# Performance work log

Hardware: AMD Instinct MI355X
Metric: run time of the kernel (lower is better)

The kernel has to match this reference:

```python
import jax, jax.numpy as jnp
import numpy as np

# Geometry constants fixed by the source's index arithmetic
GRID_P, GRID_Q, NUM_ANCH = 60, 40, 9   # p = (i//9)%60, q = i//(60*9), sr = i%9
N = GRID_P * GRID_Q * NUM_ANCH          # 21600 anchors per image
K = 1000                                # top-K candidates kept before NMS
MAX_BOXES = 18                          # fixed output boxes per image
THRESH = 0.5                            # NMS overlap threshold
BATCH = 64


def setup_inputs() -> dict:
    key = jax.random.key(0)
    k1, k2 = jax.random.split(key)
    x = jax.random.normal(k1, (BATCH, N, 6), dtype=jnp.float32)
    # anchor boxes (x, y, w, h); keep w,h strictly positive and away from 0
    anchor_boxes = jax.random.uniform(k2, (GRID_P, GRID_Q, NUM_ANCH, 4),
                                      dtype=jnp.float32, minval=0.05, maxval=1.0)
    return {"x": x, "anchor_boxes": anchor_boxes}


def _per_sample(ypred, anchors):
    scores, order = jax.lax.top_k(ypred[:, 0], K)          # descending, matches tf.argsort DESC [:1000]
    p = (order // NUM_ANCH) % GRID_P
    q = order // (GRID_P * NUM_ANCH)
    sr = order % NUM_ANCH
    a = anchors[p, q, sr]                                   # [K, 4] (xa, ya, wa, ha)
    regr = ypred[order, 2:6]                                # [K, 4] (dx, dy, dw, dh)
    xc = regr[:, 0] * a[:, 2] + a[:, 0]
    yc = regr[:, 1] * a[:, 3] + a[:, 1]
    w = a[:, 2] * jnp.exp(regr[:, 2])
    h = a[:, 3] * jnp.exp(regr[:, 3])
    cand = jnp.stack([xc, yc, w, h, scores], axis=-1)       # [K, 5] xywh+score

    # xywh -> xyxy for overlap computation (as in non_max_suppression_fast)
    x1 = xc - 0.5 * w; x2 = xc + 0.5 * w
    y1 = yc - 0.5 * h; y2 = yc + 0.5 * h
    area = (x2 - x1) * (y2 - y1)                            # [K]

    # pairwise intersection; overlap[i, j] = inter(i, j) / area(j)  (source divides by
    # the area of the lower-scored candidate, NOT the union -- kept faithfully)
    xx1 = jnp.maximum(x1[:, None], x1[None, :])
    yy1 = jnp.maximum(y1[:, None], y1[None, :])
    xx2 = jnp.minimum(x2[:, None], x2[None, :])
    yy2 = jnp.minimum(y2[:, None], y2[None, :])
    iw = jnp.maximum(0.0, xx2 - xx1)
    ih = jnp.maximum(0.0, yy2 - yy1)
    sup = (iw * ih / area[None, :]) > THRESH                # [K, K] bool

    # greedy NMS over candidates in descending-score order
    jrange = jnp.arange(K)
    def body(i, keep):
        return keep & ~(keep[i] & sup[i] & (jrange > i))
    keep = jax.lax.fori_loop(0, K, body, jnp.ones((K,), dtype=bool))

    # pack first MAX_BOXES kept boxes into fixed-shape output
    ranks = jnp.cumsum(keep) - 1                            # position among kept
    valid = keep & (ranks < MAX_BOXES)
    picked = jnp.zeros((MAX_BOXES, 5), cand.dtype).at[
        jnp.where(valid, ranks, MAX_BOXES)
    ].set(jnp.where(valid[:, None], cand, 0.0), mode='drop')

    # pad with top-scored decoded boxes if fewer than MAX_BOXES survive NMS
    n = jnp.minimum(jnp.sum(keep), MAX_BOXES)
    j = jnp.arange(MAX_BOXES)
    pad = cand[jnp.clip(j - n, 0, K - 1)]
    return jnp.where((j < n)[:, None], picked, pad)         # [MAX_BOXES, 5]


def reference(x, anchor_boxes):
    return jax.vmap(lambda y: _per_sample(y, anchor_boxes))(x)  # [B, 18, 5]
```

## Files before the change

kernel.cpp:

```cpp
#include <hip/hip_runtime.h>

#define NELEM 21600
#define KSEL 1000
#define MAXB 18
#define NT 1024
#define CAP 2048
#define NCHUNK 4
#define CHUNK (NELEM / NCHUNK)
#define NFULL 21
#define NTAIL (NELEM - NFULL * NT)

typedef unsigned long long ull;

__device__ __forceinline__ unsigned fkey(float f) {
  unsigned u = __float_as_uint(f);
  return (u & 0x80000000u) ? ~u : (u | 0x80000000u);
}
__device__ __forceinline__ float unfkey(unsigned k) {
  unsigned u = (k & 0x80000000u) ? (k ^ 0x80000000u) : ~k;
  return __uint_as_float(u);
}

__global__ __launch_bounds__(NT) void k1_scan(
    const float* __restrict__ x, unsigned* __restrict__ gkeys,
    unsigned* __restrict__ ghist) {
  const int blk = blockIdx.x;
  const int s = blk / NCHUNK, c = blk % NCHUNK;
  const int t = threadIdx.x;
  const float* xb = x + (size_t)s * NELEM * 6;

  __shared__ unsigned h[2048];
  h[2 * t] = 0u; h[2 * t + 1] = 0u;
  __syncthreads();

  const int base = c * CHUNK;
  unsigned key[6];
  bool on[6];
  #pragma unroll
  for (int k = 0; k < 6; ++k) {
    int o = t + (k << 10);
    on[k] = o < CHUNK;
    int e = base + (on[k] ? o : 0);
    key[k] = fkey(xb[(size_t)e * 6]);
  }
  #pragma unroll
  for (int k = 0; k < 6; ++k) {
    if (on[k]) {
      int e = base + t + (k << 10);
      gkeys[(size_t)s * NELEM + e] = key[k];
      atomicAdd(&h[key[k] >> 21], 1u);
    }
  }
  __syncthreads();
  unsigned* gh = ghist + (size_t)blk * 2048;
  gh[2 * t] = h[2 * t];
  gh[2 * t + 1] = h[2 * t + 1];
}

__device__ void select_bucket(const unsigned* hist, unsigned target,
                              volatile unsigned* chunkSuf,
                              unsigned* outB, unsigned* outCnt, unsigned* outAbove) {
  const int tid = threadIdx.x;
  const int w = tid >> 6, l = tid & 63;
  unsigned h1 = hist[w * 128 + 2 * l + 1];
  unsigned s = hist[w * 128 + 2 * l] + h1;
  #pragma unroll
  for (int d = 1; d < 64; d <<= 1) {
    unsigned t = __shfl_down(s, d);
    if (l + d < 64) s += t;
  }
  if (l == 0) chunkSuf[w] = s;
  __syncthreads();
  if (w == 0) {
    unsigned ct = (l < 16) ? chunkSuf[l] : 0u;
    unsigned cs = ct;
    #pragma unroll
    for (int d = 1; d < 16; d <<= 1) {
      unsigned t = __shfl_down(cs, d);
      if (l + d < 16) cs += t;
    }
    if (l < 16) chunkSuf[l] = cs - ct;
  }
  __syncthreads();
  unsigned base = chunkSuf[w];
  unsigned sufE = s + base;
  unsigned sN = __shfl_down(s, 1);
  unsigned sufN = ((l < 63) ? sN : 0u) + base;
  unsigned geOdd = sufN + h1;
  if (sufE >= target && geOdd < target) { *outB = w * 128u + 2u * l;     *outCnt = sufE;  *outAbove = geOdd; }
  if (geOdd >= target && sufN < target) { *outB = w * 128u + 2u * l + 1; *outCnt = geOdd; *outAbove = sufN;  }
  __syncthreads();
}

__global__ __launch_bounds__(NT, 4) void k2_select(
    const float* __restrict__ x, const float* __restrict__ anch,
    const unsigned* __restrict__ gkeys, const unsigned* __restrict__ ghist,
    float* __restrict__ out) {
  const int s = blockIdx.x;
  const int tid = threadIdx.x;
  const float* xb = x + (size_t)s * NELEM * 6;
  const unsigned* ks = gkeys + (size_t)s * NELEM;

  __shared__ unsigned hist[2048];
  __shared__ unsigned chunkSuf[16];
  __shared__ ull selPk[CAP];
  __shared__ float bX1[KSEL], bY1[KSEL], bX2[KSEL], bY2[KSEL], bAr[KSEL];
  __shared__ unsigned sB, sCnt, sAbove;
  __shared__ unsigned baseKey;
  __shared__ unsigned cnt;
  __shared__ int keptRank[MAXB];
  __shared__ int numKept;

  unsigned kv[NFULL];
  #pragma unroll
  for (int u = 0; u < NFULL; ++u) kv[u] = ks[tid + (u << 10)];
  unsigned ktail = 0u;
  const bool hastail = tid < NTAIL;
  if (hastail) ktail = ks[tid + NFULL * NT];
  asm volatile("" :
      "+v"(kv[0]), "+v"(kv[1]), "+v"(kv[2]), "+v"(kv[3]), "+v"(kv[4]),
      "+v"(kv[5]), "+v"(kv[6]), "+v"(kv[7]), "+v"(kv[8]), "+v"(kv[9]),
      "+v"(kv[10]), "+v"(kv[11]), "+v"(kv[12]), "+v"(kv[13]), "+v"(kv[14]),
      "+v"(kv[15]), "+v"(kv[16]), "+v"(kv[17]), "+v"(kv[18]), "+v"(kv[19]),
      "+v"(kv[20]), "+v"(ktail));

  {
    unsigned h0 = 0, h1 = 0;
    #pragma unroll
    for (int c = 0; c < NCHUNK; ++c) {
      const unsigned* gh = ghist + (size_t)(s * NCHUNK + c) * 2048;
      h0 += gh[2 * tid];
      h1 += gh[2 * tid + 1];
    }
    hist[2 * tid] = h0; hist[2 * tid + 1] = h1;
  }
  __syncthreads();
  select_bucket(hist, KSEL, chunkSuf, &sB, &sCnt, &sAbove);
  const unsigned b1 = sB, cnt1 = sCnt, above1 = sAbove;

  if (cnt1 <= CAP) {
    if (tid == 0) { baseKey = b1 << 21; cnt = 0u; }
  } else {
    hist[2 * tid] = 0u; hist[2 * tid + 1] = 0u;
    __syncthreads();
    #pragma unroll
    for (int u = 0; u < NFULL; ++u)
      if ((kv[u] >> 21) == b1) atomicAdd(&hist[(kv[u] >> 10) & 0x7FFu], 1u);
    if (hastail && (ktail >> 21) == b1) atomicAdd(&hist[(ktail >> 10) & 0x7FFu], 1u);
    __syncthreads();
    select_bucket(hist, KSEL - above1, chunkSuf, &sB, &sCnt, &sAbove);
    if (tid == 0) { baseKey = (b1 << 21) | (sB << 10); cnt = 0u; }
  }
  __syncthreads();

  const unsigned TB = baseKey;
  #pragma unroll
  for (int u = 0; u < NFULL; ++u) {
    if (kv[u] >= TB) {
      unsigned p = atomicAdd(&cnt, 1u);
      unsigned i = (unsigned)(tid + (u << 10));
      if (p < CAP) selPk[p] = ((ull)kv[u] << 32) | (unsigned)(~i);
    }
  }
  if (hastail && ktail >= TB) {
    unsigned p = atomicAdd(&cnt, 1u);
    unsigned i = (unsigned)(tid + NFULL * NT);
    if (p < CAP) selPk[p] = ((ull)ktail << 32) | (unsigned)(~i);
  }
  __syncthreads();
  const unsigned realCnt = (cnt < CAP) ? cnt : CAP;
  for (unsigned i = realCnt + tid; i < CAP; i += NT) selPk[i] = 0ull;
  __syncthreads();

  {
    const int w = tid >> 6, L = tid & 63;
    const int ea = (w << 7) | (L << 1);
    ull a = selPk[ea], bb = selPk[ea + 1];
    #pragma unroll
    for (unsigned k = 2; k <= 128; k <<= 1) {
      #pragma unroll
      for (unsigned j = k >> 1; j >= 2; j >>= 1) {
        bool up = ((ea & k) == 0);
        bool lower = ((ea & j) == 0);
        bool takeMax = (up == lower);
        ull oa = __shfl_xor(a, (int)(j >> 1));
        ull ob = __shfl_xor(bb, (int)(j >> 1));
        a  = takeMax ? (a  > oa ? a  : oa) : (a  < oa ? a  : oa);
        bb = takeMax ? (bb > ob ? bb : ob) : (bb < ob ? bb : ob);
      }
      bool up = ((ea & k) == 0);
      ull mx = a > bb ? a : bb, mn = a > bb ? bb : a;
      a = up ? mx : mn; bb = up ? mn : mx;
    }
    selPk[ea] = a; selPk[ea + 1] = bb;
    __syncthreads();
    for (unsigned k = 256; k <= 2048; k <<= 1) {
      for (unsigned j = k >> 1; j >= 128; j >>= 1) {
        unsigned p = (unsigned)tid;
        unsigned vi = ((p & ~(j - 1)) << 1) | (p & (j - 1));
        unsigned li = vi | j;
        ull av = selPk[vi], cv = selPk[li];
        bool doswap = ((vi & k) == 0) ? (av < cv) : (av > cv);
        if (doswap) { selPk[vi] = cv; selPk[li] = av; }
        __syncthreads();
      }
      a = selPk[ea]; bb = selPk[ea + 1];
      bool up = (((unsigned)(w << 7) & k) == 0);
      #pragma unroll
      for (unsigned j = 64; j >= 2; j >>= 1) {
        bool lower = ((ea & j) == 0);
        bool takeMax = (up == lower);
        ull oa = __shfl_xor(a, (int)(j >> 1));
        ull ob = __shfl_xor(bb, (int)(j >> 1));
        a  = takeMax ? (a  > oa ? a  : oa) : (a  < oa ? a  : oa);
        bb = takeMax ? (bb > ob ? bb : ob) : (bb < ob ? bb : ob);
      }
      ull mx = a > bb ? a : bb, mn = a > bb ? bb : a;
      a = up ? mx : mn; bb = up ? mn : mx;
      selPk[ea] = a; selPk[ea + 1] = bb;
      __syncthreads();
    }
  }

  if (tid < KSEL) {
    unsigned idx = ~(unsigned)selPk[tid];
    const float2* e2 = (const float2*)(xb + (size_t)idx * 6 + 2);
    float2 ra = e2[0], rb = e2[1];
    unsigned pp = (idx / 9u) % 60u;
    unsigned qq = idx / 540u;
    unsigned sr = idx % 9u;
    const float* ap = anch + (((pp * 40u + qq) * 9u + sr) * 4u);
    float ax = ap[0], ay = ap[1], aw = ap[2], ah = ap[3];
    float xc = ra.x * aw + ax;
    float yc = ra.y * ah + ay;
    float w = aw * expf(rb.x);
    float h = ah * expf(rb.y);
    float x1 = xc - 0.5f * w, x2 = xc + 0.5f * w;
    float y1 = yc - 0.5f * h, y2 = yc + 0.5f * h;
    bX1[tid] = x1; bY1[tid] = y1; bX2[tid] = x2; bY2[tid] = y2;
    bAr[tid] = (x2 - x1) * (y2 - y1);
  }
  __syncthreads();

  if (tid < 64) {
    const int lane = tid;
    int nk = 0;
    float kx1 = 0.f, ky1 = 0.f, kx2 = 0.f, ky2 = 0.f;
    int krank = -1;
    for (int base = 0; base < KSEL && nk < MAXB; base += 64) {
      int c = base + lane;
      bool alive = (c < KSEL);
      int cc = alive ? c : 0;
      float x1 = bX1[cc], y1 = bY1[cc], x2 = bX2[cc], y2 = bY2[cc], ar = bAr[cc];
      for (int i = 0; i < nk; ++i) {
        float px1 = __shfl(kx1, i), py1 = __shfl(ky1, i);
        float px2 = __shfl(kx2, i), py2 = __shfl(ky2, i);
        float iw = fmaxf(fminf(x2, px2) - fmaxf(x1, px1), 0.f);
        float ih = fmaxf(fminf(y2, py2) - fmaxf(y1, py1), 0.f);
        if (iw * ih / ar > 0.5f) alive = false;
      }
      unsigned long long m = __ballot(alive);
      while (m) {
        int i = __builtin_ctzll(m);
        float px1 = __shfl(x1, i), py1 = __shfl(y1, i);
        float px2 = __shfl(x2, i), py2 = __shfl(y2, i);
        if (lane == nk) { kx1 = px1; ky1 = py1; kx2 = px2; ky2 = py2; krank = base + i; }
        ++nk;
        if (nk >= MAXB) break;
        if (alive && lane != i) {
          float iw = fmaxf(fminf(x2, px2) - fmaxf(x1, px1), 0.f);
          float ih = fmaxf(fminf(y2, py2) - fmaxf(y1, py1), 0.f);
          if (iw * ih / ar > 0.5f) alive = false;
        }
        if (lane == i) alive = false;
        m = __ballot(alive);
      }
    }
    if (lane == 0) numKept = nk;
    if (lane < nk) keptRank[lane] = krank;
  }
  __syncthreads();

  const int n = numKept;
  if (tid < MAXB) {
    int j = tid;
    int r = (j < n) ? keptRank[j] : (j - n);
    ull pk = selPk[r];
    unsigned idx = ~(unsigned)pk;
    float sc = unfkey((unsigned)(pk >> 32));
    const float2* e2 = (const float2*)(xb + (size_t)idx * 6 + 2);
    float2 ra = e2[0], rb = e2[1];
    unsigned pp = (idx / 9u) % 60u;
    unsigned qq = idx / 540u;
    unsigned sr = idx % 9u;
    const float* ap = anch + (((pp * 40u + qq) * 9u + sr) * 4u);
    float ax = ap[0], ay = ap[1], aw = ap[2], ah = ap[3];
    float xc = ra.x * aw + ax;
    float yc = ra.y * ah + ay;
    float w = aw * expf(rb.x);
    float h = ah * expf(rb.y);
    float* o = out + s * (MAXB * 5) + j * 5;
    o[0] = xc; o[1] = yc; o[2] = w; o[3] = h; o[4] = sc;
  }
}

extern "C" void kernel_launch(void* const* d_in, const int* in_sizes, int n_in,
                              void* d_out, int out_size, void* d_ws, size_t ws_size,
                              hipStream_t stream) {
  const float* x = (const float*)d_in[0];
  const float* anch = (const float*)d_in[1];
  float* out = (float*)d_out;
  const int B = in_sizes[0] / (NELEM * 6);
  unsigned* ghist = (unsigned*)d_ws;
  unsigned* gkeys = ghist + (size_t)B * NCHUNK * 2048;
  k1_scan<<<dim3(B * NCHUNK), dim3(NT), 0, stream>>>(x, gkeys, ghist);
  k2_select<<<dim3(B), dim3(NT), 0, stream>>>(x, anch, gkeys, ghist, out);
}
```

Measured before the change: 65.66 us.

## Aggregate compaction atomics per wave, add 1024-wide sort path, rework NMS loop

Compaction now uses one wave-level atomicAdd per ballot instead of a per-element atomic. The second-level histogram refinement is triggered above 1024 candidates so a smaller single-element-per-thread bitonic sort can run over 1024 entries, with an intra-wave shuffle phase and shared-memory phases. The NMS phase is rewritten so each lane holds 16 consecutive candidates in registers and the next kept box is found by a wave-wide min reduction; each kept box is then tested against all survivors. This trades extra histogram passes and more per-iteration register work for fewer atomics and less sort traffic.

```diff
diff --git a/kernel.cpp b/kernel.cpp
--- a/kernel.cpp
+++ b/kernel.cpp
@@ -138,9 +138,7 @@
   select_bucket(hist, KSEL, chunkSuf, &sB, &sCnt, &sAbove);
   const unsigned b1 = sB, cnt1 = sCnt, above1 = sAbove;
 
-  if (cnt1 <= CAP) {
-    if (tid == 0) { baseKey = b1 << 21; cnt = 0u; }
-  } else {
+  if (cnt1 > 1024) {
     hist[2 * tid] = 0u; hist[2 * tid + 1] = 0u;
     __syncthreads();
     #pragma unroll
@@ -150,16 +148,28 @@
     __syncthreads();
     select_bucket(hist, KSEL - above1, chunkSuf, &sB, &sCnt, &sAbove);
     if (tid == 0) { baseKey = (b1 << 21) | (sB << 10); cnt = 0u; }
+  } else {
+    if (tid == 0) { baseKey = b1 << 21; cnt = 0u; }
   }
   __syncthreads();
 
   const unsigned TB = baseKey;
+  const int lw = tid & 63;
   #pragma unroll
   for (int u = 0; u < NFULL; ++u) {
-    if (kv[u] >= TB) {
-      unsigned p = atomicAdd(&cnt, 1u);
-      unsigned i = (unsigned)(tid + (u << 10));
-      if (p < CAP) selPk[p] = ((ull)kv[u] << 32) | (unsigned)(~i);
+    bool pred = kv[u] >= TB;
+    ull mask = __ballot(pred);
+    if (mask) {
+      int leader = __builtin_ctzll(mask);
+      unsigned total = (unsigned)__popcll(mask);
+      unsigned basep = 0;
+      if (lw == leader) basep = atomicAdd(&cnt, total);
+      basep = __shfl(basep, leader);
+      if (pred) {
+        unsigned p = basep + (unsigned)__popcll(mask & ((1ull << lw) - 1ull));
+        unsigned i = (unsigned)(tid + (u << 10));
+        if (p < CAP) selPk[p] = ((ull)kv[u] << 32) | (unsigned)(~i);
+      }
     }
   }
   if (hastail && ktail >= TB) {
@@ -169,10 +179,52 @@
   }
   __syncthreads();
   const unsigned realCnt = (cnt < CAP) ? cnt : CAP;
-  for (unsigned i = realCnt + tid; i < CAP; i += NT) selPk[i] = 0ull;
-  __syncthreads();
-
-  {
+  const unsigned P = (realCnt <= 1024u) ? 1024u : 2048u;
+  for (unsigned i = realCnt + tid; i < P; i += NT) selPk[i] = 0ull;
+  __syncthreads();
+
+  if (P == 1024u) {
+    ull a = selPk[tid];
+    #pragma unroll
+    for (unsigned k = 2; k <= 64; k <<= 1) {
+      #pragma unroll
+      for (unsigned j = k >> 1; j >= 1; j >>= 1) {
+        bool up = ((tid & k) == 0);
+        bool lower = ((tid & j) == 0);
+        bool takeMax = (up == lower);
+        ull o = __shfl_xor(a, (int)j);
+        a = takeMax ? (a > o ? a : o) : (a < o ? a : o);
+      }
+    }
+    selPk[tid] = a;
+    __syncthreads();
+    for (unsigned k = 128; k <= 1024; k <<= 1) {
+      for (unsigned j = k >> 1; j >= 64; j >>= 1) {
+        if (tid < 512) {
+          unsigned p = (unsigned)tid;
+          unsigned vi = ((p & ~(j - 1)) << 1) | (p & (j - 1));
+          unsigned li = vi | j;
+          ull av = selPk[vi], cv = selPk[li];
+          bool doswap = ((vi & k) == 0) ? (av < cv) : (av > cv);
+          if (doswap) { selPk[vi] = cv; selPk[li] = av; }
+        }
+        __syncthreads();
+      }
+      a = selPk[tid];
+      {
+        bool up = ((tid & k) == 0);
+        #pragma unroll
+        for (unsigned j = 32; j >= 1; j >>= 1) {
+          bool lower = ((tid & j) == 0);
+          bool takeMax = (up == lower);
+          ull o = __shfl_xor(a, (int)j);
+          a = takeMax ? (a > o ? a : o) : (a < o ? a : o);
+        }
+      }
+      selPk[tid] = a;
+      __syncthreads();
+    }
+  } else {
     const int w = tid >> 6, L = tid & 63;
     const int ea = (w << 7) | (L << 1);
     ull a = selPk[ea], bb = selPk[ea + 1];
@@ -244,40 +296,42 @@
 
   if (tid < 64) {
     const int lane = tid;
+    float X1[16], Y1[16], X2[16], Y2[16], AR[16];
+    unsigned alive = 0u;
+    #pragma unroll
+    for (int ss = 0; ss < 16; ++ss) {
+      int r = lane * 16 + ss;
+      bool ok = r < KSEL;
+      int rr = ok ? r : 0;
+      X1[ss] = bX1[rr]; Y1[ss] = bY1[rr];
+      X2[ss] = bX2[rr]; Y2[ss] = bY2[rr]; AR[ss] = bAr[rr];
+      alive |= (ok ? 1u : 0u) << ss;
+    }
     int nk = 0;
-    float kx1 = 0.f, ky1 = 0.f, kx2 = 0.f, ky2 = 0.f;
-    int krank = -1;
-    for (int base = 0; base < KSEL && nk < MAXB; base += 64) {
-      int c = base + lane;
-      bool alive = (c < KSEL);
-      int cc = alive ? c : 0;
-      float x1 = bX1[cc], y1 = bY1[cc], x2 = bX2[cc], y2 = bY2[cc], ar = bAr[cc];
-      for (int i = 0; i < nk; ++i) {
-        float px1 = __shfl(kx1, i), py1 = __shfl(ky1, i);
-        float px2 = __shfl(kx2, i), py2 = __shfl(ky2, i);
-        float iw = fmaxf(fminf(x2, px2) - fmaxf(x1, px1), 0.f);
-        float ih = fmaxf(fminf(y2, py2) - fmaxf(y1, py1), 0.f);
-        if (iw * ih / ar > 0.5f) alive = false;
-      }
-      unsigned long long m = __ballot(alive);
-      while (m) {
-        int i = __builtin_ctzll(m);
-        float px1 = __shfl(x1, i), py1 = __shfl(y1, i);
-        float px2 = __shfl(x2, i), py2 = __shfl(y2, i);
-        if (lane == nk) { kx1 = px1; ky1 = py1; kx2 = px2; ky2 = py2; krank = base + i; }
-        ++nk;
-        if (nk >= MAXB) break;
-        if (alive && lane != i) {
-          float iw = fmaxf(fminf(x2, px2) - fmaxf(x1, px1), 0.f);
-          float ih = fmaxf(fminf(y2, py2) - fmaxf(y1, py1), 0.f);
-          if (iw * ih / ar > 0.5f) alive = false;
+    while (nk < MAXB) {
+      int local = alive ? (lane * 16 + (int)__builtin_ctz(alive)) : (1 << 30);
+      int m = local;
+      #pragma unroll
+      for (int d = 1; d < 64; d <<= 1) {
+        int o = __shfl_xor(m, d);
+        m = o < m ? o : m;
+      }
+      if (m >= (1 << 30)) break;
+      if (lane == 0) keptRank[nk] = m;
+      float wx1 = bX1[m], wy1 = bY1[m], wx2 = bX2[m], wy2 = bY2[m];
+      ++nk;
+      if (alive) {
+        #pragma unroll
+        for (int ss = 0; ss < 16; ++ss) {
+          if (alive & (1u << ss)) {
+            float iw = fmaxf(fminf(X2[ss], wx2) - fmaxf(X1[ss], wx1), 0.f);
+            float ih = fmaxf(fminf(Y2[ss], wy2) - fmaxf(Y1[ss], wy1), 0.f);
+            if (iw * ih / AR[ss] > 0.5f) alive &= ~(1u << ss);
+          }
         }
-        if (lane == i) alive = false;
-        m = __ballot(alive);
       }
     }
     if (lane == 0) numKept = nk;
-    if (lane < nk) keptRank[lane] = krank;
   }
   __syncthreads();
 
```

Measured after the change: 60.93 us. 7.2% less time.
